# Kernel optimization log

Hardware: AMD Instinct MI355X
Metric: run time of the kernel (lower is better)

The kernel has to match this reference:

```python
import jax, jax.numpy as jnp
import numpy as np

NUM_GROUPS = 32
EPS = 1e-6


def setup_inputs() -> dict:
    key = jax.random.key(0)
    ks = jax.random.split(key, 4)
    B, C, H, W = 16, 512, 32, 32
    x = jax.random.normal(ks[0], (B, C, H, W), dtype=jnp.float32)
    norm_w = jnp.ones((C,), dtype=jnp.float32)
    norm_b = jnp.zeros((C,), dtype=jnp.float32)
    qkv_w = jax.random.normal(ks[1], (3 * C, C), dtype=jnp.float32) * (1.0 / np.sqrt(C))
    qkv_b = jnp.zeros((3 * C,), dtype=jnp.float32)
    proj_w = jax.random.normal(ks[2], (C, C), dtype=jnp.float32) * (1.0 / np.sqrt(C))
    proj_b = jnp.zeros((C,), dtype=jnp.float32)
    return {"x": x, "norm_w": norm_w, "norm_b": norm_b, "qkv_w": qkv_w,
            "qkv_b": qkv_b, "proj_w": proj_w, "proj_b": proj_b}


def _group_norm(x, w, b):
    B, C, H, W = x.shape
    g = NUM_GROUPS
    xg = x.reshape(B, g, C // g, H * W)
    mu = xg.mean(axis=(2, 3), keepdims=True)
    var = xg.var(axis=(2, 3), keepdims=True)
    xn = (xg - mu) * jax.lax.rsqrt(var + EPS)
    xn = xn.reshape(B, C, H, W)
    return xn * w[None, :, None, None] + b[None, :, None, None]


def reference(x, norm_w, norm_b, qkv_w, qkv_b, proj_w, proj_b):
    B, C, H, W = x.shape
    h = _group_norm(x, norm_w, norm_b)
    # 1x1 conv == channel GEMM
    qkv = jnp.einsum('oc,bchw->bohw', qkv_w, h) + qkv_b[None, :, None, None]
    q, k, v = jnp.split(qkv, 3, axis=1)
    N = H * W
    q = q.reshape(B, C, N)  # (b, c, n)
    k = k.reshape(B, C, N)
    v = v.reshape(B, C, N)
    scale = jnp.asarray(C, x.dtype) ** -0.5
    attn = jnp.einsum('bci,bcj->bij', q, k) * scale  # (b, Nq, Nk)
    attn = jax.nn.softmax(attn, axis=2)
    o = jnp.einsum('bcj,bij->bci', v, attn).reshape(B, C, H, W)
    out = jnp.einsum('oc,bchw->bohw', proj_w, o) + proj_b[None, :, None, None]
    return x + out
```

## Files before the change

### kernel.cpp

```cpp
#include <hip/hip_runtime.h>

typedef unsigned short u16;
typedef __bf16 bf16x8 __attribute__((ext_vector_type(8)));
typedef float f32x4 __attribute__((ext_vector_type(4)));


__device__ __forceinline__ u16 f2bf(float f) {
  union { float f; unsigned u; } v; v.f = f;
  return (u16)((v.u + 0x7fffu + ((v.u >> 16) & 1u)) >> 16);
}

__device__ __forceinline__ float bf2f(u16 x) {
  union { unsigned u; float f; } v; v.u = ((unsigned)x) << 16; return v.f;
}

__device__ __forceinline__ f32x4 mfma16(bf16x8 a, bf16x8 b, f32x4 c) {
  return __builtin_amdgcn_mfma_f32_16x16x32_bf16(a, b, c, 0, 0, 0);
}

__device__ __forceinline__ void stage_tile(const u16* __restrict__ src, size_t ld,
                                           u16* lds, int wv, int lane) {
#pragma unroll
  for (int h2 = 0; h2 < 2; h2++) {
    int rbase = wv * 32 + h2 * 16;
    int row = rbase + (lane >> 2);
    int segd = (lane & 3) ^ ((row >> 1) & 3);
    __builtin_amdgcn_global_load_lds(
        (const __attribute__((address_space(1))) void*)(src + (size_t)row * ld + segd * 8),
        (__attribute__((address_space(3))) void*)(lds + rbase * 32),
        16, 0, 0);
  }
}

__device__ __forceinline__ bf16x8 ldsfrag(const u16* lds, int row, int rowq) {
  int q = rowq ^ ((row >> 1) & 3);
  return *(const bf16x8*)(lds + row * 32 + q * 8);
}

__global__ __launch_bounds__(256) void gn_stats(const float* __restrict__ x,
                                                float* __restrict__ mean,
                                                float* __restrict__ rstd) {
  int bg = blockIdx.x;
  const float4* p = (const float4*)(x + (size_t)bg * 16384);
  float s = 0.f, ss = 0.f;
  for (int i = threadIdx.x; i < 4096; i += 256) {
    float4 v = p[i];
    s  += v.x + v.y + v.z + v.w;
    ss += v.x*v.x + v.y*v.y + v.z*v.z + v.w*v.w;
  }
  for (int d = 32; d; d >>= 1) { s += __shfl_down(s, d); ss += __shfl_down(ss, d); }
  __shared__ float ls[4], lss[4];
  int wave = threadIdx.x >> 6;
  if ((threadIdx.x & 63) == 0) { ls[wave] = s; lss[wave] = ss; }
  __syncthreads();
  if (threadIdx.x == 0) {
    s = ls[0] + ls[1] + ls[2] + ls[3];
    ss = lss[0] + lss[1] + lss[2] + lss[3];
    float m = s * (1.f / 16384.f);
    float var = ss * (1.f / 16384.f) - m * m;
    mean[bg] = m;
    rstd[bg] = rsqrtf(var + 1e-6f);
  }
}

__global__ __launch_bounds__(256) void cast_bf16(const float* __restrict__ src,
                                                 u16* __restrict__ dst, int n) {
  int i = (blockIdx.x * 256 + threadIdx.x) * 4;
  if (i < n) {
    float4 v = *(const float4*)(src + i);
    dst[i] = f2bf(v.x); dst[i+1] = f2bf(v.y); dst[i+2] = f2bf(v.z); dst[i+3] = f2bf(v.w);
  }
}

__global__ __launch_bounds__(256) void gn_apply(const float* __restrict__ x,
                                                const float* __restrict__ mean,
                                                const float* __restrict__ rstd,
                                                const float* __restrict__ gw,
                                                const float* __restrict__ gb,
                                                u16* __restrict__ h) {
  __shared__ u16 tile[64][72];
  int b = blockIdx.z, c0 = blockIdx.y * 64, n0 = blockIdx.x * 64;
  int t = threadIdx.x;
  int cc = t >> 2, ns = (t & 3) * 16;
  int c = c0 + cc, g = c >> 4;
  float m = mean[b * 32 + g], r = rstd[b * 32 + g];
  float w = gw[c] * r;
  float bb = gb[c] - m * w;
  const float* xr = x + (((size_t)(b * 512 + c)) << 10) + n0 + ns;
#pragma unroll
  for (int u = 0; u < 16; u += 4) {
    float4 v = *(const float4*)(xr + u);
    tile[cc][ns + u + 0] = f2bf(v.x * w + bb);
    tile[cc][ns + u + 1] = f2bf(v.y * w + bb);
    tile[cc][ns + u + 2] = f2bf(v.z * w + bb);
    tile[cc][ns + u + 3] = f2bf(v.w * w + bb);
  }
  __syncthreads();
  int nn = t >> 2, cs = (t & 3) * 16;
  u16* hr = h + (((size_t)(b * 1024 + n0 + nn)) << 9) + c0 + cs;
  u16 vals[16];
#pragma unroll
  for (int u = 0; u < 16; u++) vals[u] = tile[cs + u][nn];
  *(uint4*)hr = *(uint4*)vals;
  *(uint4*)(hr + 8) = *(uint4*)(vals + 8);
}

__global__ __launch_bounds__(256) void gemm_qkv(const u16* __restrict__ A,
                                                const u16* __restrict__ Bn,
                                                const float* __restrict__ bias,
                                                u16* __restrict__ q_nc,
                                                u16* __restrict__ k_nc,
                                                u16* __restrict__ v) {
  __shared__ u16 sA[128 * 32];
  __shared__ u16 sB[128 * 32];
  int bid = blockIdx.x;
  int xcd = bid & 7, r = bid >> 3;
  int mb = r % 12, nb = xcd * 16 + r / 12;
  int m0 = mb * 128, n0 = nb * 128;
  int t = threadIdx.x, wave = t >> 6, lane = t & 63;
  int wm = wave >> 1, wn = wave & 1;
  int col = lane & 15, rowq = lane >> 4;
  f32x4 acc[4][4];
#pragma unroll
  for (int i = 0; i < 4; i++)
#pragma unroll
    for (int j = 0; j < 4; j++) acc[i][j] = (f32x4){0.f, 0.f, 0.f, 0.f};

  for (int k0 = 0; k0 < 512; k0 += 32) {
    __syncthreads();
    stage_tile(A + (size_t)m0 * 512 + k0, 512, sA, wave, lane);
    stage_tile(Bn + (size_t)n0 * 512 + k0, 512, sB, wave, lane);
    __syncthreads();
    bf16x8 af[4], bfr[4];
#pragma unroll
    for (int i = 0; i < 4; i++) af[i] = ldsfrag(sA, wm * 64 + i * 16 + col, rowq);
#pragma unroll
    for (int j = 0; j < 4; j++) bfr[j] = ldsfrag(sB, wn * 64 + j * 16 + col, rowq);
#pragma unroll
    for (int i = 0; i < 4; i++)
#pragma unroll
      for (int j = 0; j < 4; j++) acc[i][j] = mfma16(af[i], bfr[j], acc[i][j]);
  }
  if (mb < 8) {
    u16* dst = (mb < 4) ? q_nc : k_nc;
#pragma unroll
    for (int i = 0; i < 4; i++)
#pragma unroll
      for (int j = 0; j < 4; j++) {
        int o = m0 + wm * 64 + i * 16 + rowq * 4;
        int bn = n0 + wn * 64 + j * 16 + col;
        u16 tmp[4];
#pragma unroll
        for (int rr = 0; rr < 4; rr++) tmp[rr] = f2bf(acc[i][j][rr] + bias[o + rr]);
        *(uint2*)(dst + (size_t)bn * 512 + (o & 511)) = *(uint2*)tmp;
      }
  } else {
#pragma unroll
    for (int i = 0; i < 4; i++)
#pragma unroll
      for (int j = 0; j < 4; j++)
#pragma unroll
        for (int rr = 0; rr < 4; rr++) {
          int o = m0 + wm * 64 + i * 16 + rowq * 4 + rr;
          int bn = n0 + wn * 64 + j * 16 + col;
          v[(size_t)(o & 511) * 16384 + bn] = f2bf(acc[i][j][rr] + bias[o]);
        }
  }
}

__global__ __launch_bounds__(256) void gemm_s(const u16* __restrict__ q_nc,
                                              const u16* __restrict__ k_nc,
                                              u16* __restrict__ E) {
  __shared__ u16 sA[128 * 32];
  __shared__ u16 sB[128 * 32];
  int bid = blockIdx.x;
  int xcd = bid & 7, r2 = bid >> 3;
  int b = xcd * 2 + (r2 & 1);
  int tile = r2 >> 1;
  int m0 = (tile >> 3) * 128, n0 = (tile & 7) * 128;
  const u16* A  = q_nc + ((size_t)b << 10) * 512;
  const u16* Bn = k_nc + ((size_t)b << 10) * 512;
  int t = threadIdx.x, wave = t >> 6, lane = t & 63;
  int wm = wave >> 1, wn = wave & 1;
  int col = lane & 15, rowq = lane >> 4;
  f32x4 acc[4][4];
#pragma unroll
  for (int i = 0; i < 4; i++)
#pragma unroll
    for (int j = 0; j < 4; j++) acc[i][j] = (f32x4){0.f, 0.f, 0.f, 0.f};

  for (int k0 = 0; k0 < 512; k0 += 32) {
    __syncthreads();
    stage_tile(A + (size_t)m0 * 512 + k0, 512, sA, wave, lane);
    stage_tile(Bn + (size_t)n0 * 512 + k0, 512, sB, wave, lane);
    __syncthreads();
    bf16x8 af[4], bfr[4];
#pragma unroll
    for (int i = 0; i < 4; i++) af[i] = ldsfrag(sA, wm * 64 + i * 16 + col, rowq);
#pragma unroll
    for (int j = 0; j < 4; j++) bfr[j] = ldsfrag(sB, wn * 64 + j * 16 + col, rowq);
#pragma unroll
    for (int i = 0; i < 4; i++)
#pragma unroll
      for (int j = 0; j < 4; j++) acc[i][j] = mfma16(af[i], bfr[j], acc[i][j]);
  }
  u16* Eb = E + ((size_t)b << 20);
  const float scale = 0.04419417382415922f;
#pragma unroll
  for (int i = 0; i < 4; i++)
#pragma unroll
    for (int j = 0; j < 4; j++) {
      int ii = m0 + wm * 64 + i * 16 + rowq * 4;
      int jj = n0 + wn * 64 + j * 16 + col;
#pragma unroll
      for (int rr = 0; rr < 4; rr++)
        Eb[(size_t)(ii + rr) * 1024 + jj] = f2bf(__expf(acc[i][j][rr] * scale));
    }
}

__global__ __launch_bounds__(256) void row_inv(const u16* __restrict__ E,
                                               float* __restrict__ inv) {
  int row = blockIdx.x * 4 + (threadIdx.x >> 6);
  int lane = threadIdx.x & 63;
  const u16* er = E + (size_t)row * 1024 + lane * 16;
  uint4 a = *(const uint4*)er;
  uint4 c = *(const uint4*)(er + 8);
  float s = 0.f;
  unsigned ws[8] = {a.x, a.y, a.z, a.w, c.x, c.y, c.z, c.w};
#pragma unroll
  for (int u = 0; u < 8; u++) {
    union { unsigned u; float f; } lo, hi;
    lo.u = ws[u] << 16; hi.u = ws[u] & 0xffff0000u;
    s += lo.f + hi.f;
  }
#pragma unroll
  for (int d = 1; d < 64; d <<= 1) s += __shfl_xor(s, d);
  if (lane == 0) inv[row] = 1.0f / s;
}

__global__ __launch_bounds__(256) void gemm_pv(const u16* __restrict__ E,
                                               const u16* __restrict__ v,
                                               const float* __restrict__ inv,
                                               u16* __restrict__ o_nc) {
  __shared__ u16 sA[128 * 32];
  __shared__ u16 sB[128 * 32];
  int bid = blockIdx.x;
  int xcd = bid & 7, r2 = bid >> 3;
  int b = xcd * 2 + (r2 & 1);
  int tile = r2 >> 1;
  int m0 = (tile >> 2) * 128, n0 = (tile & 3) * 128;
  const u16* A = E + ((size_t)b << 20);
  int t = threadIdx.x, wave = t >> 6, lane = t & 63;
  int wm = wave >> 1, wn = wave & 1;
  int col = lane & 15, rowq = lane >> 4;
  f32x4 acc[4][4];
#pragma unroll
  for (int i = 0; i < 4; i++)
#pragma unroll
    for (int j = 0; j < 4; j++) acc[i][j] = (f32x4){0.f, 0.f, 0.f, 0.f};

  for (int k0 = 0; k0 < 1024; k0 += 32) {
    __syncthreads();
    stage_tile(A + (size_t)m0 * 1024 + k0, 1024, sA, wave, lane);
    stage_tile(v + (size_t)n0 * 16384 + ((size_t)b << 10) + k0, 16384, sB, wave, lane);
    __syncthreads();
    bf16x8 af[4], bfr[4];
#pragma unroll
    for (int i = 0; i < 4; i++) af[i] = ldsfrag(sA, wm * 64 + i * 16 + col, rowq);
#pragma unroll
    for (int j = 0; j < 4; j++) bfr[j] = ldsfrag(sB, wn * 64 + j * 16 + col, rowq);
#pragma unroll
    for (int i = 0; i < 4; i++)
#pragma unroll
      for (int j = 0; j < 4; j++) acc[i][j] = mfma16(af[i], bfr[j], acc[i][j]);
  }
#pragma unroll
  for (int i = 0; i < 4; i++)
#pragma unroll
    for (int j = 0; j < 4; j++)
#pragma unroll
      for (int rr = 0; rr < 4; rr++) {
        int ii = m0 + wm * 64 + i * 16 + rowq * 4 + rr;
        int cc = n0 + wn * 64 + j * 16 + col;
        float sc = inv[(b << 10) + ii];
        o_nc[(((size_t)(b * 1024 + ii)) << 9) + cc] = f2bf(acc[i][j][rr] * sc);
      }
}

__global__ __launch_bounds__(256) void gemm_proj(const u16* __restrict__ A,
                                                 const u16* __restrict__ Bn,
                                                 const float* __restrict__ bias,
                                                 const float* __restrict__ xres,
                                                 float* __restrict__ outp) {
  __shared__ u16 sA[128 * 32];
  __shared__ u16 sB[128 * 32];
  int bid = blockIdx.x;
  int xcd = bid & 7, r = bid >> 3;
  int mb = r & 3, nb = xcd * 16 + (r >> 2);
  int m0 = mb * 128, n0 = nb * 128;
  int t = threadIdx.x, wave = t >> 6, lane = t & 63;
  int wm = wave >> 1, wn = wave & 1;
  int col = lane & 15, rowq = lane >> 4;
  f32x4 acc[4][4];
#pragma unroll
  for (int i = 0; i < 4; i++)
#pragma unroll
    for (int j = 0; j < 4; j++) acc[i][j] = (f32x4){0.f, 0.f, 0.f, 0.f};

  for (int k0 = 0; k0 < 512; k0 += 32) {
    __syncthreads();
    stage_tile(A + (size_t)m0 * 512 + k0, 512, sA, wave, lane);
    stage_tile(Bn + (size_t)n0 * 512 + k0, 512, sB, wave, lane);
    __syncthreads();
    bf16x8 af[4], bfr[4];
#pragma unroll
    for (int i = 0; i < 4; i++) af[i] = ldsfrag(sA, wm * 64 + i * 16 + col, rowq);
#pragma unroll
    for (int j = 0; j < 4; j++) bfr[j] = ldsfrag(sB, wn * 64 + j * 16 + col, rowq);
#pragma unroll
    for (int i = 0; i < 4; i++)
#pragma unroll
      for (int j = 0; j < 4; j++) acc[i][j] = mfma16(af[i], bfr[j], acc[i][j]);
  }
#pragma unroll
  for (int i = 0; i < 4; i++)
#pragma unroll
    for (int j = 0; j < 4; j++)
#pragma unroll
      for (int rr = 0; rr < 4; rr++) {
        int co = m0 + wm * 64 + i * 16 + rowq * 4 + rr;
        int bn = n0 + wn * 64 + j * 16 + col;
        int bb = bn >> 10, n = bn & 1023;
        size_t oi = (((size_t)(bb * 512 + co)) << 10) + n;
        outp[oi] = acc[i][j][rr] + bias[co] + xres[oi];
      }
}

extern "C" void kernel_launch(void* const* d_in, const int* in_sizes, int n_in,
                              void* d_out, int out_size, void* d_ws, size_t ws_size,
                              hipStream_t stream) {
  const float* x      = (const float*)d_in[0];
  const float* norm_w = (const float*)d_in[1];
  const float* norm_b = (const float*)d_in[2];
  const float* qkv_w  = (const float*)d_in[3];
  const float* qkv_b  = (const float*)d_in[4];
  const float* proj_w = (const float*)d_in[5];
  const float* proj_b = (const float*)d_in[6];
  float* out = (float*)d_out;

  char* ws = (char*)d_ws;
  size_t off = 0;
  auto alloc = [&](size_t bytes) {
    void* p = ws + off;
    off += (bytes + 255) & ~(size_t)255;
    return p;
  };
  float* mean = (float*)alloc(512 * 4);
  float* rstd = (float*)alloc(512 * 4);
  float* inv  = (float*)alloc(16384 * 4);
  u16* wq   = (u16*)alloc((size_t)1536 * 512 * 2);
  u16* wp   = (u16*)alloc((size_t)512 * 512 * 2);
  u16* h    = (u16*)alloc((size_t)16384 * 512 * 2);
  u16* q_nc = (u16*)alloc((size_t)16384 * 512 * 2);
  u16* k_nc = (u16*)alloc((size_t)16384 * 512 * 2);
  u16* v    = (u16*)alloc((size_t)512 * 16384 * 2);
  u16* E    = (u16*)alloc((size_t)16 * 1024 * 1024 * 2);
  u16* o_nc = h;
  (void)in_sizes; (void)n_in; (void)out_size; (void)ws_size;

  gn_stats<<<512, 256, 0, stream>>>(x, mean, rstd);
  cast_bf16<<<(1536 * 512) / 1024, 256, 0, stream>>>(qkv_w, wq, 1536 * 512);
  cast_bf16<<<(512 * 512) / 1024, 256, 0, stream>>>(proj_w, wp, 512 * 512);
  gn_apply<<<dim3(16, 8, 16), 256, 0, stream>>>(x, mean, rstd, norm_w, norm_b, h);
  gemm_qkv<<<1536, 256, 0, stream>>>(wq, h, qkv_b, q_nc, k_nc, v);
  gemm_s<<<1024, 256, 0, stream>>>(q_nc, k_nc, E);
  row_inv<<<4096, 256, 0, stream>>>(E, inv);
  gemm_pv<<<512, 256, 0, stream>>>(E, v, inv, o_nc);
  gemm_proj<<<512, 256, 0, stream>>>(wp, o_nc, proj_b, x, out);
}
```

Measured before the change: 153.1 us.

## Unify GEMMs into double-buffered 512-thread core with larger tiles

Replaces the four single-buffered GEMM loops with a shared templated core. The core uses 512-thread blocks, 64-wide K steps, a two-stage LDS double buffer with explicit vmcnt waits, and s_setprio around the MFMA bursts. Tiles grow to 128x256 or 256x256 and the grids shrink to match, so each tile is loaded fewer times and global loads overlap with compute. The cost is much larger LDS use (96-128KB), which limits occupancy to one block per CU, and fewer blocks to balance across the 256 CUs.

Result: faster. 140.4 us (-8.3%).

```diff
diff --git a/kernel.cpp b/kernel.cpp
--- a/kernel.cpp
+++ b/kernel.cpp
@@ -4,37 +4,94 @@
 typedef __bf16 bf16x8 __attribute__((ext_vector_type(8)));
 typedef float f32x4 __attribute__((ext_vector_type(4)));
 
+#define AS1 __attribute__((address_space(1)))
+#define AS3 __attribute__((address_space(3)))
+
 
 __device__ __forceinline__ u16 f2bf(float f) {
   union { float f; unsigned u; } v; v.f = f;
   return (u16)((v.u + 0x7fffu + ((v.u >> 16) & 1u)) >> 16);
 }
 
-__device__ __forceinline__ float bf2f(u16 x) {
-  union { unsigned u; float f; } v; v.u = ((unsigned)x) << 16; return v.f;
-}
-
 __device__ __forceinline__ f32x4 mfma16(bf16x8 a, bf16x8 b, f32x4 c) {
   return __builtin_amdgcn_mfma_f32_16x16x32_bf16(a, b, c, 0, 0, 0);
 }
 
-__device__ __forceinline__ void stage_tile(const u16* __restrict__ src, size_t ld,
-                                           u16* lds, int wv, int lane) {
-#pragma unroll
-  for (int h2 = 0; h2 < 2; h2++) {
-    int rbase = wv * 32 + h2 * 16;
-    int row = rbase + (lane >> 2);
-    int segd = (lane & 3) ^ ((row >> 1) & 3);
+template<int ROUNDS>
+__device__ __forceinline__ void stage_mat(const u16* __restrict__ src, int ld,
+                                          u16* lds, int wave, int lane) {
+#pragma unroll
+  for (int rnd = 0; rnd < ROUNDS; rnd++) {
+    int rbase = rnd * 64 + wave * 8;
+    int row = rbase + (lane >> 3);
+    int slot = (lane & 7) ^ (row & 7);
     __builtin_amdgcn_global_load_lds(
-        (const __attribute__((address_space(1))) void*)(src + (size_t)row * ld + segd * 8),
-        (__attribute__((address_space(3))) void*)(lds + rbase * 32),
-        16, 0, 0);
-  }
-}
-
-__device__ __forceinline__ bf16x8 ldsfrag(const u16* lds, int row, int rowq) {
-  int q = rowq ^ ((row >> 1) & 3);
-  return *(const bf16x8*)(lds + row * 32 + q * 8);
+        (const AS1 void*)(src + (size_t)row * ld + slot * 8),
+        (AS3 void*)(lds + rbase * 64), 16, 0, 0);
+  }
+}
+
+template<int M_REP, int NT>
+__device__ __forceinline__ void gemm_core(const u16* __restrict__ A, int lda,
+                                          const u16* __restrict__ B, int ldb,
+                                          u16* lds, f32x4 (&acc)[M_REP][4],
+                                          int wave, int lane) {
+  constexpr int BM = M_REP * 32;
+  constexpr int AR = BM / 64;
+  constexpr int ATILE = BM * 64;
+  constexpr int VM = AR + 4;
+  u16* sA0 = lds;
+  u16* sA1 = lds + ATILE;
+  u16* sB0 = lds + 2 * ATILE;
+  u16* sB1 = lds + 2 * ATILE + 16384;
+  int wm = wave >> 2, wn = wave & 3;
+  int col = lane & 15, rq = lane >> 4;
+#pragma unroll
+  for (int m = 0; m < M_REP; m++)
+#pragma unroll
+    for (int n = 0; n < 4; n++) acc[m][n] = (f32x4){0.f, 0.f, 0.f, 0.f};
+
+  stage_mat<AR>(A, lda, sA0, wave, lane);
+  stage_mat<4>(B, ldb, sB0, wave, lane);
+  stage_mat<AR>(A + 64, lda, sA1, wave, lane);
+  stage_mat<4>(B + 64, ldb, sB1, wave, lane);
+
+  for (int t = 0; t < NT; t++) {
+    u16* cA = (t & 1) ? sA1 : sA0;
+    u16* cB = (t & 1) ? sB1 : sB0;
+    if (t < NT - 1) {
+      asm volatile("s_waitcnt vmcnt(%0)" :: "i"(VM) : "memory");
+    } else {
+      asm volatile("s_waitcnt vmcnt(0)" ::: "memory");
+    }
+    __builtin_amdgcn_sched_barrier(0);
+    __builtin_amdgcn_s_barrier();
+    __builtin_amdgcn_sched_barrier(0);
+    __builtin_amdgcn_s_setprio(1);
+#pragma unroll
+    for (int kk = 0; kk < 2; kk++) {
+      bf16x8 bfr[4];
+#pragma unroll
+      for (int n = 0; n < 4; n++) {
+        int row = wn * 64 + n * 16 + col;
+        bfr[n] = *(const bf16x8*)(cB + row * 64 + ((kk * 4 + rq) ^ (row & 7)) * 8);
+      }
+#pragma unroll
+      for (int m = 0; m < M_REP; m++) {
+        int row = wm * (BM / 2) + m * 16 + col;
+        bf16x8 af = *(const bf16x8*)(cA + row * 64 + ((kk * 4 + rq) ^ (row & 7)) * 8);
+#pragma unroll
+        for (int n = 0; n < 4; n++) acc[m][n] = mfma16(af, bfr[n], acc[m][n]);
+      }
+    }
+    __builtin_amdgcn_s_setprio(0);
+    __builtin_amdgcn_sched_barrier(0);
+    __builtin_amdgcn_s_barrier();
+    if (t + 2 < NT) {
+      stage_mat<AR>(A + (size_t)(t + 2) * 64, lda, cA, wave, lane);
+      stage_mat<4>(B + (size_t)(t + 2) * 64, ldb, cB, wave, lane);
+    }
+  }
 }
 
 __global__ __launch_bounds__(256) void gn_stats(const float* __restrict__ x,
@@ -105,49 +162,30 @@
   *(uint4*)(hr + 8) = *(uint4*)(vals + 8);
 }
 
-__global__ __launch_bounds__(256) void gemm_qkv(const u16* __restrict__ A,
-                                                const u16* __restrict__ Bn,
-                                                const float* __restrict__ bias,
-                                                u16* __restrict__ q_nc,
-                                                u16* __restrict__ k_nc,
-                                                u16* __restrict__ v) {
-  __shared__ u16 sA[128 * 32];
-  __shared__ u16 sB[128 * 32];
+__global__ __launch_bounds__(512, 1) void gemm_qkv(const u16* __restrict__ A,
+                                                   const u16* __restrict__ Bn,
+                                                   const float* __restrict__ bias,
+                                                   u16* __restrict__ q_nc,
+                                                   u16* __restrict__ k_nc,
+                                                   u16* __restrict__ v) {
+  __shared__ u16 lds[49152];
   int bid = blockIdx.x;
   int xcd = bid & 7, r = bid >> 3;
-  int mb = r % 12, nb = xcd * 16 + r / 12;
-  int m0 = mb * 128, n0 = nb * 128;
+  int mb = r % 12, nb = xcd * 8 + r / 12;
+  int m0 = mb * 128, n0 = nb * 256;
   int t = threadIdx.x, wave = t >> 6, lane = t & 63;
-  int wm = wave >> 1, wn = wave & 1;
-  int col = lane & 15, rowq = lane >> 4;
+  int wm = wave >> 2, wn = wave & 3;
+  int col = lane & 15, rq = lane >> 4;
   f32x4 acc[4][4];
-#pragma unroll
-  for (int i = 0; i < 4; i++)
-#pragma unroll
-    for (int j = 0; j < 4; j++) acc[i][j] = (f32x4){0.f, 0.f, 0.f, 0.f};
-
-  for (int k0 = 0; k0 < 512; k0 += 32) {
-    __syncthreads();
-    stage_tile(A + (size_t)m0 * 512 + k0, 512, sA, wave, lane);
-    stage_tile(Bn + (size_t)n0 * 512 + k0, 512, sB, wave, lane);
-    __syncthreads();
-    bf16x8 af[4], bfr[4];
-#pragma unroll
-    for (int i = 0; i < 4; i++) af[i] = ldsfrag(sA, wm * 64 + i * 16 + col, rowq);
-#pragma unroll
-    for (int j = 0; j < 4; j++) bfr[j] = ldsfrag(sB, wn * 64 + j * 16 + col, rowq);
-#pragma unroll
-    for (int i = 0; i < 4; i++)
-#pragma unroll
-      for (int j = 0; j < 4; j++) acc[i][j] = mfma16(af[i], bfr[j], acc[i][j]);
-  }
+  gemm_core<4, 8>(A + (size_t)m0 * 512, 512, Bn + (size_t)n0 * 512, 512,
+                  lds, acc, wave, lane);
   if (mb < 8) {
     u16* dst = (mb < 4) ? q_nc : k_nc;
 #pragma unroll
     for (int i = 0; i < 4; i++)
 #pragma unroll
       for (int j = 0; j < 4; j++) {
-        int o = m0 + wm * 64 + i * 16 + rowq * 4;
+        int o = m0 + wm * 64 + i * 16 + rq * 4;
         int bn = n0 + wn * 64 + j * 16 + col;
         u16 tmp[4];
 #pragma unroll
@@ -161,56 +199,36 @@
       for (int j = 0; j < 4; j++)
 #pragma unroll
         for (int rr = 0; rr < 4; rr++) {
-          int o = m0 + wm * 64 + i * 16 + rowq * 4 + rr;
+          int o = m0 + wm * 64 + i * 16 + rq * 4 + rr;
           int bn = n0 + wn * 64 + j * 16 + col;
           v[(size_t)(o & 511) * 16384 + bn] = f2bf(acc[i][j][rr] + bias[o]);
         }
   }
 }
 
-__global__ __launch_bounds__(256) void gemm_s(const u16* __restrict__ q_nc,
-                                              const u16* __restrict__ k_nc,
-                                              u16* __restrict__ E) {
-  __shared__ u16 sA[128 * 32];
-  __shared__ u16 sB[128 * 32];
+__global__ __launch_bounds__(512, 1) void gemm_s(const u16* __restrict__ q_nc,
+                                                 const u16* __restrict__ k_nc,
+                                                 u16* __restrict__ E) {
+  __shared__ u16 lds[65536];
   int bid = blockIdx.x;
-  int xcd = bid & 7, r2 = bid >> 3;
-  int b = xcd * 2 + (r2 & 1);
-  int tile = r2 >> 1;
-  int m0 = (tile >> 3) * 128, n0 = (tile & 7) * 128;
-  const u16* A  = q_nc + ((size_t)b << 10) * 512;
-  const u16* Bn = k_nc + ((size_t)b << 10) * 512;
+  int xcd = bid & 7, r = bid >> 3;
+  int b = xcd * 2 + (r & 1);
+  int tile = r >> 1;
+  int m0 = (tile >> 2) * 256, n0 = (tile & 3) * 256;
   int t = threadIdx.x, wave = t >> 6, lane = t & 63;
-  int wm = wave >> 1, wn = wave & 1;
-  int col = lane & 15, rowq = lane >> 4;
-  f32x4 acc[4][4];
-#pragma unroll
-  for (int i = 0; i < 4; i++)
-#pragma unroll
-    for (int j = 0; j < 4; j++) acc[i][j] = (f32x4){0.f, 0.f, 0.f, 0.f};
-
-  for (int k0 = 0; k0 < 512; k0 += 32) {
-    __syncthreads();
-    stage_tile(A + (size_t)m0 * 512 + k0, 512, sA, wave, lane);
-    stage_tile(Bn + (size_t)n0 * 512 + k0, 512, sB, wave, lane);
-    __syncthreads();
-    bf16x8 af[4], bfr[4];
-#pragma unroll
-    for (int i = 0; i < 4; i++) af[i] = ldsfrag(sA, wm * 64 + i * 16 + col, rowq);
-#pragma unroll
-    for (int j = 0; j < 4; j++) bfr[j] = ldsfrag(sB, wn * 64 + j * 16 + col, rowq);
-#pragma unroll
-    for (int i = 0; i < 4; i++)
-#pragma unroll
-      for (int j = 0; j < 4; j++) acc[i][j] = mfma16(af[i], bfr[j], acc[i][j]);
-  }
+  int wm = wave >> 2, wn = wave & 3;
+  int col = lane & 15, rq = lane >> 4;
+  f32x4 acc[8][4];
+  const u16* A  = q_nc + ((size_t)(b * 1024 + m0)) * 512;
+  const u16* Bn = k_nc + ((size_t)(b * 1024 + n0)) * 512;
+  gemm_core<8, 8>(A, 512, Bn, 512, lds, acc, wave, lane);
   u16* Eb = E + ((size_t)b << 20);
   const float scale = 0.04419417382415922f;
 #pragma unroll
-  for (int i = 0; i < 4; i++)
+  for (int i = 0; i < 8; i++)
 #pragma unroll
     for (int j = 0; j < 4; j++) {
-      int ii = m0 + wm * 64 + i * 16 + rowq * 4;
+      int ii = m0 + wm * 128 + i * 16 + rq * 4;
       int jj = n0 + wn * 64 + j * 16 + col;
 #pragma unroll
       for (int rr = 0; rr < 4; rr++)
@@ -238,97 +256,59 @@
   if (lane == 0) inv[row] = 1.0f / s;
 }
 
-__global__ __launch_bounds__(256) void gemm_pv(const u16* __restrict__ E,
-                                               const u16* __restrict__ v,
-                                               const float* __restrict__ inv,
-                                               u16* __restrict__ o_nc) {
-  __shared__ u16 sA[128 * 32];
-  __shared__ u16 sB[128 * 32];
+__global__ __launch_bounds__(512, 1) void gemm_pv(const u16* __restrict__ E,
+                                                  const u16* __restrict__ v,
+                                                  const float* __restrict__ inv,
+                                                  u16* __restrict__ o_nc) {
+  __shared__ u16 lds[49152];
   int bid = blockIdx.x;
-  int xcd = bid & 7, r2 = bid >> 3;
-  int b = xcd * 2 + (r2 & 1);
-  int tile = r2 >> 1;
-  int m0 = (tile >> 2) * 128, n0 = (tile & 3) * 128;
-  const u16* A = E + ((size_t)b << 20);
+  int xcd = bid & 7, r = bid >> 3;
+  int b = xcd * 2 + (r & 1);
+  int tile = r >> 1;
+  int m0 = (tile >> 1) * 128, n0 = (tile & 1) * 256;
   int t = threadIdx.x, wave = t >> 6, lane = t & 63;
-  int wm = wave >> 1, wn = wave & 1;
-  int col = lane & 15, rowq = lane >> 4;
+  int wm = wave >> 2, wn = wave & 3;
+  int col = lane & 15, rq = lane >> 4;
   f32x4 acc[4][4];
+  const u16* A  = E + ((size_t)b << 20) + (size_t)m0 * 1024;
+  const u16* Bn = v + (size_t)n0 * 16384 + ((size_t)b << 10);
+  gemm_core<4, 16>(A, 1024, Bn, 16384, lds, acc, wave, lane);
 #pragma unroll
   for (int i = 0; i < 4; i++)
 #pragma unroll
-    for (int j = 0; j < 4; j++) acc[i][j] = (f32x4){0.f, 0.f, 0.f, 0.f};
-
-  for (int k0 = 0; k0 < 1024; k0 += 32) {
-    __syncthreads();
-    stage_tile(A + (size_t)m0 * 1024 + k0, 1024, sA, wave, lane);
-    stage_tile(v + (size_t)n0 * 16384 + ((size_t)b << 10) + k0, 16384, sB, wave, lane);
-    __syncthreads();
-    bf16x8 af[4], bfr[4];
-#pragma unroll
-    for (int i = 0; i < 4; i++) af[i] = ldsfrag(sA, wm * 64 + i * 16 + col, rowq);
-#pragma unroll
-    for (int j = 0; j < 4; j++) bfr[j] = ldsfrag(sB, wn * 64 + j * 16 + col, rowq);
-#pragma unroll
-    for (int i = 0; i < 4; i++)
-#pragma unroll
-      for (int j = 0; j < 4; j++) acc[i][j] = mfma16(af[i], bfr[j], acc[i][j]);
-  }
-#pragma unroll
-  for (int i = 0; i < 4; i++)
-#pragma unroll
     for (int j = 0; j < 4; j++)
 #pragma unroll
       for (int rr = 0; rr < 4; rr++) {
-        int ii = m0 + wm * 64 + i * 16 + rowq * 4 + rr;
+        int ii = m0 + wm * 64 + i * 16 + rq * 4 + rr;
         int cc = n0 + wn * 64 + j * 16 + col;
         float sc = inv[(b << 10) + ii];
         o_nc[(((size_t)(b * 1024 + ii)) << 9) + cc] = f2bf(acc[i][j][rr] * sc);
       }
 }
 
-__global__ __launch_bounds__(256) void gemm_proj(const u16* __restrict__ A,
-                                                 const u16* __restrict__ Bn,
-                                                 const float* __restrict__ bias,
-                                                 const float* __restrict__ xres,
-                                                 float* __restrict__ outp) {
-  __shared__ u16 sA[128 * 32];
-  __shared__ u16 sB[128 * 32];
+__global__ __launch_bounds__(512, 1) void gemm_proj(const u16* __restrict__ A,
+                                                    const u16* __restrict__ Bn,
+                                                    const float* __restrict__ bias,
+                                                    const float* __restrict__ xres,
+                                                    float* __restrict__ outp) {
+  __shared__ u16 lds[49152];
   int bid = blockIdx.x;
   int xcd = bid & 7, r = bid >> 3;
-  int mb = r & 3, nb = xcd * 16 + (r >> 2);
-  int m0 = mb * 128, n0 = nb * 128;
+  int mb = r % 4, nb = xcd * 8 + r / 4;
+  int m0 = mb * 128, n0 = nb * 256;
   int t = threadIdx.x, wave = t >> 6, lane = t & 63;
-  int wm = wave >> 1, wn = wave & 1;
-  int col = lane & 15, rowq = lane >> 4;
+  int wm = wave >> 2, wn = wave & 3;
+  int col = lane & 15, rq = lane >> 4;
   f32x4 acc[4][4];
+  gemm_core<4, 8>(A + (size_t)m0 * 512, 512, Bn + (size_t)n0 * 512, 512,
+                  lds, acc, wave, lane);
 #pragma unroll
   for (int i = 0; i < 4; i++)
 #pragma unroll
-    for (int j = 0; j < 4; j++) acc[i][j] = (f32x4){0.f, 0.f, 0.f, 0.f};
-
-  for (int k0 = 0; k0 < 512; k0 += 32) {
-    __syncthreads();
-    stage_tile(A + (size_t)m0 * 512 + k0, 512, sA, wave, lane);
-    stage_tile(Bn + (size_t)n0 * 512 + k0, 512, sB, wave, lane);
-    __syncthreads();
-    bf16x8 af[4], bfr[4];
-#pragma unroll
-    for (int i = 0; i < 4; i++) af[i] = ldsfrag(sA, wm * 64 + i * 16 + col, rowq);
-#pragma unroll
-    for (int j = 0; j < 4; j++) bfr[j] = ldsfrag(sB, wn * 64 + j * 16 + col, rowq);
-#pragma unroll
-    for (int i = 0; i < 4; i++)
-#pragma unroll
-      for (int j = 0; j < 4; j++) acc[i][j] = mfma16(af[i], bfr[j], acc[i][j]);
-  }
-#pragma unroll
-  for (int i = 0; i < 4; i++)
-#pragma unroll
     for (int j = 0; j < 4; j++)
 #pragma unroll
       for (int rr = 0; rr < 4; rr++) {
-        int co = m0 + wm * 64 + i * 16 + rowq * 4 + rr;
+        int co = m0 + wm * 64 + i * 16 + rq * 4 + rr;
         int bn = n0 + wn * 64 + j * 16 + col;
         int bb = bn >> 10, n = bn & 1023;
         size_t oi = (((size_t)(bb * 512 + co)) << 10) + n;
@@ -372,9 +352,9 @@
   cast_bf16<<<(1536 * 512) / 1024, 256, 0, stream>>>(qkv_w, wq, 1536 * 512);
   cast_bf16<<<(512 * 512) / 1024, 256, 0, stream>>>(proj_w, wp, 512 * 512);
   gn_apply<<<dim3(16, 8, 16), 256, 0, stream>>>(x, mean, rstd, norm_w, norm_b, h);
-  gemm_qkv<<<1536, 256, 0, stream>>>(wq, h, qkv_b, q_nc, k_nc, v);
-  gemm_s<<<1024, 256, 0, stream>>>(q_nc, k_nc, E);
+  gemm_qkv<<<768, 512, 0, stream>>>(wq, h, qkv_b, q_nc, k_nc, v);
+  gemm_s<<<256, 512, 0, stream>>>(q_nc, k_nc, E);
   row_inv<<<4096, 256, 0, stream>>>(E, inv);
-  gemm_pv<<<512, 256, 0, stream>>>(E, v, inv, o_nc);
-  gemm_proj<<<512, 256, 0, stream>>>(wp, o_nc, proj_b, x, out);
-}
+  gemm_pv<<<256, 512, 0, stream>>>(E, v, inv, o_nc);
+  gemm_proj<<<256, 512, 0, stream>>>(wp, o_nc, proj_b, x, out);
+}
```
